# Kernel tuning notes

Hardware: AMD Instinct MI355X
Metric: run time of the kernel (lower is better)

## Reference

```python
import jax, jax.numpy as jnp
import numpy as np

B, N, D, S = 64, 1024, 8, 16
SPARSE_PROB = 0.1


def setup_inputs() -> dict:
    key = jax.random.key(0)
    k_x, k_m, k_ws, k_bd, k_wd, k_bs = jax.random.split(key, 6)
    x = jax.random.normal(k_x, (B, N, D, S), dtype=jnp.float32)
    # conexao='esparsa': (rand < 0.1).float() buffer, exactly like _criar_matriz_conexao
    matriz_conexao = (jax.random.uniform(k_m, (N, N)) < SPARSE_PROB).astype(jnp.float32)
    # Stacked per-neuron parameters of NeuronioDendritico
    w_syn = jax.random.normal(k_ws, (N, D, S), dtype=jnp.float32) * 0.1   # synapse weights
    b_dend = jax.random.normal(k_bd, (N, D), dtype=jnp.float32) * 0.1     # dendrite bias
    w_dend = jax.random.normal(k_wd, (N, D), dtype=jnp.float32) * 0.1     # dendrite->soma weights
    b_soma = jax.random.normal(k_bs, (N,), dtype=jnp.float32) * 0.1       # soma bias
    return {"x": x, "matriz_conexao": matriz_conexao, "w_syn": w_syn,
            "b_dend": b_dend, "w_dend": w_dend, "b_soma": b_soma}


def reference(x, matriz_conexao, w_syn, b_dend, w_dend, b_soma):
    # Connectivity mixing across neurons (conexao != 'densa'):
    # torch.einsum('bids,oi->bods', x, matriz_conexao)
    xm = jnp.einsum('bids,oi->bods', x, matriz_conexao)  # [B, N, D, S]
    # Fused batched version of the Python loop over n_neurons:
    # each dendrite: tanh(sum_s w*x + b)
    dend = jnp.tanh(jnp.einsum('bnds,nds->bnd', xm, w_syn) + b_dend[None])  # [B, N, D]
    # soma: weighted sum of dendritic outputs + bias -> sigmoid spike
    soma = jnp.einsum('bnd,nd->bn', dend, w_dend) + b_soma[None]            # [B, N]
    spikes = jax.nn.sigmoid(soma)
    return spikes
```

## Files before the change

### kernel.cpp

```cpp
#include <hip/hip_runtime.h>
#include <hip/hip_bf16.h>

#define BB 64
#define NN 1024
#define DD 8
#define SS 16
#define DS 128

typedef __attribute__((ext_vector_type(8))) short short8;
typedef __attribute__((ext_vector_type(4))) float floatx4;

typedef __attribute__((address_space(1))) const unsigned int glds_src;
typedef __attribute__((address_space(3))) unsigned int glds_dst;

static __device__ __forceinline__ unsigned short f2bf(float f) {
    unsigned int u = __float_as_uint(f);
    unsigned int r = (u + 0x7FFFu + ((u >> 16) & 1u)) >> 16;
    return (unsigned short)r;
}

__global__ void prepass(const float* __restrict__ x, unsigned short* __restrict__ xT,
                        const float* __restrict__ M, unsigned short* __restrict__ Mb) {
    __shared__ float tile[64 * 68];
    const int t = threadIdx.x;

    if (blockIdx.x < 1024) {
        int i = (blockIdx.x * 256 + t) * 4;
        float4 v = *(const float4*)(M + i);
        unsigned int p0 = (unsigned int)f2bf(v.x) | ((unsigned int)f2bf(v.y) << 16);
        unsigned int p1 = (unsigned int)f2bf(v.z) | ((unsigned int)f2bf(v.w) << 16);
        *(uint2*)(Mb + i) = make_uint2(p0, p1);
        return;
    }

    const int bid = blockIdx.x - 1024;
    const int i0 = (bid & 15) * 64;
    const int c0 = ((bid >> 4) & 1) * 64;
    const int b  = bid >> 5;
    const float* xb = x + (size_t)b * (NN * DS);

#pragma unroll
    for (int jj = 0; jj < 4; ++jj) {
        int il = (t >> 4) + jj * 16;
        int cl = (t & 15) * 4;
        float4 v = *(const float4*)(xb + (size_t)(i0 + il) * DS + c0 + cl);
        *(float4*)(tile + il * 68 + cl) = v;
    }
    __syncthreads();
    int cr  = t >> 2;
    int iq  = (t & 3) * 16;
    int rot = (t & 3) * 2;
    unsigned int p[8];
#pragma unroll
    for (int j = 0; j < 8; ++j) {
        int jp = (j + rot) & 7;
        unsigned short lo = f2bf(tile[(iq + 2 * jp + 0) * 68 + cr]);
        unsigned short hi = f2bf(tile[(iq + 2 * jp + 1) * 68 + cr]);
        p[jp] = (unsigned int)lo | ((unsigned int)hi << 16);
    }
    unsigned short* dst = xT + (size_t)b * (NN * DS) + (size_t)(c0 + cr) * NN + i0 + iq;
    *(uint4*)(dst + 0) = make_uint4(p[0], p[1], p[2], p[3]);
    *(uint4*)(dst + 8) = make_uint4(p[4], p[5], p[6], p[7]);
}

__global__ __launch_bounds__(256, 2) void gemm_fused(
    const unsigned short* __restrict__ Mb,
    const unsigned short* __restrict__ xT,
    const float* __restrict__ w_syn,
    const float* __restrict__ b_dend,
    const float* __restrict__ w_dend,
    const float* __restrict__ b_soma,
    float* __restrict__ out)
{
    __shared__ __align__(16) unsigned short As[128 * 128];
    __shared__ __align__(16) unsigned short Bs[128 * 128];
    __shared__ float ex[128 * 2];

    const int t      = threadIdx.x;
    const int b      = blockIdx.x;
    const int o_base = blockIdx.y * 128;

    const char* AgB = (const char*)(Mb + (size_t)o_base * NN);
    const char* BgB = (const char*)(xT + (size_t)b * (NN * DS));

    const int lane = t & 63;
    const int w    = t >> 6;
    const int wr   = (w >> 1) * 64;
    const int wc   = (w & 1) * 64;
    const int lm   = lane & 15;
    const int kq   = lane >> 4;

    int off[8], ldsb[8];
#pragma unroll
    for (int j = 0; j < 8; ++j) {
        const int row = (w * 8 + j) * 4 + (lane >> 4);
        const int sg  = (lane & 15) ^ (row & 15);
        off[j]  = row * (NN * 2) + sg * 16;
        ldsb[j] = (w * 8 + j) * 1024;
    }

    floatx4 acc[4][4] = {};

    for (int kt = 0; kt < 8; ++kt) {
        const int kb = kt * 256;
        __syncthreads();
#pragma unroll
        for (int j = 0; j < 8; ++j) {
            __builtin_amdgcn_global_load_lds((glds_src*)(AgB + off[j] + kb),
                                             (glds_dst*)((char*)As + ldsb[j]), 16, 0, 0);
            __builtin_amdgcn_global_load_lds((glds_src*)(BgB + off[j] + kb),
                                             (glds_dst*)((char*)Bs + ldsb[j]), 16, 0, 0);
        }
        __syncthreads();
#pragma unroll
        for (int ks = 0; ks < 4; ++ks) {
            short8 af[4], bf[4];
            const int g = (((ks * 4 + kq) ^ lm) * 8);
#pragma unroll
            for (int r = 0; r < 4; ++r)
                af[r] = *(const short8*)(As + (wr + r * 16 + lm) * 128 + g);
#pragma unroll
            for (int c = 0; c < 4; ++c)
                bf[c] = *(const short8*)(Bs + (wc + c * 16 + lm) * 128 + g);
#pragma unroll
            for (int r = 0; r < 4; ++r)
#pragma unroll
                for (int c = 0; c < 4; ++c)
                    acc[r][c] = __builtin_amdgcn_mfma_f32_16x16x32_bf16(af[r], bf[c], acc[r][c], 0, 0, 0);
        }
    }

    float keep[4];
#pragma unroll
    for (int r = 0; r < 4; ++r) {
#pragma unroll
        for (int rg = 0; rg < 4; ++rg) {
            const int o = o_base + wr + r * 16 + kq * 4 + rg;
#pragma unroll
            for (int c = 0; c < 4; ++c) {
                const int d = (w & 1) * 4 + c;
                float p = acc[r][c][rg] * w_syn[o * DS + d * SS + lm];
                p += __shfl_xor(p, 1);
                p += __shfl_xor(p, 2);
                p += __shfl_xor(p, 4);
                p += __shfl_xor(p, 8);
                if (lm == r * 4 + rg) keep[c] = p;
            }
        }
    }
    {
        const int o_loc = wr + (lm >> 2) * 16 + kq * 4 + (lm & 3);
        const int o     = o_base + o_loc;
        float part = 0.f;
#pragma unroll
        for (int c = 0; c < 4; ++c) {
            const int d = (w & 1) * 4 + c;
            float pre = keep[c] + b_dend[o * DD + d];
            part += tanhf(pre) * w_dend[o * DD + d];
        }
        ex[o_loc * 2 + (w & 1)] = part;
    }
    __syncthreads();
    if (t < 128) {
        float soma = ex[t * 2] + ex[t * 2 + 1] + b_soma[o_base + t];
        out[(size_t)b * NN + o_base + t] = 1.f / (1.f + __expf(-soma));
    }
}

extern "C" void kernel_launch(void* const* d_in, const int* in_sizes, int n_in,
                              void* d_out, int out_size, void* d_ws, size_t ws_size,
                              hipStream_t stream) {
    const float* x      = (const float*)d_in[0];
    const float* M      = (const float*)d_in[1];
    const float* w_syn  = (const float*)d_in[2];
    const float* b_dend = (const float*)d_in[3];
    const float* w_dend = (const float*)d_in[4];
    const float* b_soma = (const float*)d_in[5];
    float* out = (float*)d_out;

    unsigned short* xT = (unsigned short*)d_ws;
    unsigned short* Mb = xT + (size_t)BB * NN * DS;

    prepass   <<<dim3(1024 + 2048), 256, 0, stream>>>(x, xT, M, Mb);
    gemm_fused<<<dim3(BB, NN / 128), 256, 0, stream>>>(Mb, xT, w_syn, b_dend, w_dend, b_soma, out);
}
```

Before: 108.5 us.

## Retile fused GEMM to 256x128 with 8 waves and triple-buffered LDS pipeline

Each block now covers 256 output neurons with 512 threads (8 waves in a 2x4 layout), and the K loop uses 64-wide steps with a three-stage LDS buffer fed by async global_load_lds. Loads for stage kt+2 are split into two halves and issued during the MFMA phases, with explicit vmcnt waits, barriers and setprio around the MFMA blocks. The goal is to overlap global loads with matrix math and to halve the re-reads of the per-batch xT tile. This raises LDS use to about 144KB per block and register pressure, which may cut occupancy, and the handwritten wait counts are fragile.

Result: slower. 111.4 us (+2.6%).

```diff
diff --git a/kernel.cpp b/kernel.cpp
--- a/kernel.cpp
+++ b/kernel.cpp
@@ -63,7 +63,7 @@
     *(uint4*)(dst + 8) = make_uint4(p[4], p[5], p[6], p[7]);
 }
 
-__global__ __launch_bounds__(256, 2) void gemm_fused(
+__global__ __launch_bounds__(512, 2) void gemm_fused(
     const unsigned short* __restrict__ Mb,
     const unsigned short* __restrict__ xT,
     const float* __restrict__ w_syn,
@@ -72,97 +72,144 @@
     const float* __restrict__ b_soma,
     float* __restrict__ out)
 {
-    __shared__ __align__(16) unsigned short As[128 * 128];
-    __shared__ __align__(16) unsigned short Bs[128 * 128];
-    __shared__ float ex[128 * 2];
+    __shared__ __align__(16) unsigned short As[3 * 256 * 64];
+    __shared__ __align__(16) unsigned short Bs[3 * 128 * 64];
+    __shared__ float ex[256 * 4];
 
     const int t      = threadIdx.x;
     const int b      = blockIdx.x;
-    const int o_base = blockIdx.y * 128;
+    const int o_base = blockIdx.y * 256;
+
+    const int lane = t & 63;
+    const int w    = t >> 6;
+    const int wm   = w >> 2;
+    const int wn   = w & 3;
+    const int lm   = lane & 15;
+    const int kq   = lane >> 4;
 
     const char* AgB = (const char*)(Mb + (size_t)o_base * NN);
     const char* BgB = (const char*)(xT + (size_t)b * (NN * DS));
 
-    const int lane = t & 63;
-    const int w    = t >> 6;
-    const int wr   = (w >> 1) * 64;
-    const int wc   = (w & 1) * 64;
-    const int lm   = lane & 15;
-    const int kq   = lane >> 4;
-
-    int off[8], ldsb[8];
-#pragma unroll
-    for (int j = 0; j < 8; ++j) {
-        const int row = (w * 8 + j) * 4 + (lane >> 4);
-        const int sg  = (lane & 15) ^ (row & 15);
-        off[j]  = row * (NN * 2) + sg * 16;
-        ldsb[j] = (w * 8 + j) * 1024;
-    }
-
-    floatx4 acc[4][4] = {};
-
-    for (int kt = 0; kt < 8; ++kt) {
-        const int kb = kt * 256;
-        __syncthreads();
-#pragma unroll
-        for (int j = 0; j < 8; ++j) {
-            __builtin_amdgcn_global_load_lds((glds_src*)(AgB + off[j] + kb),
-                                             (glds_dst*)((char*)As + ldsb[j]), 16, 0, 0);
-            __builtin_amdgcn_global_load_lds((glds_src*)(BgB + off[j] + kb),
-                                             (glds_dst*)((char*)Bs + ldsb[j]), 16, 0, 0);
-        }
-        __syncthreads();
-#pragma unroll
-        for (int ks = 0; ks < 4; ++ks) {
-            short8 af[4], bf[4];
-            const int g = (((ks * 4 + kq) ^ lm) * 8);
-#pragma unroll
-            for (int r = 0; r < 4; ++r)
-                af[r] = *(const short8*)(As + (wr + r * 16 + lm) * 128 + g);
-#pragma unroll
-            for (int c = 0; c < 4; ++c)
-                bf[c] = *(const short8*)(Bs + (wc + c * 16 + lm) * 128 + g);
-#pragma unroll
-            for (int r = 0; r < 4; ++r)
-#pragma unroll
-                for (int c = 0; c < 4; ++c)
-                    acc[r][c] = __builtin_amdgcn_mfma_f32_16x16x32_bf16(af[r], bf[c], acc[r][c], 0, 0, 0);
-        }
-    }
-
-    float keep[4];
-#pragma unroll
-    for (int r = 0; r < 4; ++r) {
+    const int r8 = lane >> 3, l8 = lane & 7;
+    const int sg = (l8 ^ r8) * 16;
+    int offA[4], ldsA[4], offB[2], ldsB[2];
+#pragma unroll
+    for (int j = 0; j < 4; ++j) {
+        offA[j] = (w * 32 + j * 8 + r8) * (NN * 2) + sg;
+        ldsA[j] = (w * 32 + j * 8) * 128;
+    }
+#pragma unroll
+    for (int j = 0; j < 2; ++j) {
+        offB[j] = (w * 16 + j * 8 + r8) * (NN * 2) + sg;
+        ldsB[j] = (w * 16 + j * 8) * 128;
+    }
+
+#define STAGE_H0(TT, BUF) do { const int kb_ = (TT) * 128;                                            \
+    __builtin_amdgcn_global_load_lds((glds_src*)(AgB + offA[0] + kb_),                                \
+        (glds_dst*)((char*)As + (BUF) * 32768 + ldsA[0]), 16, 0, 0);                                  \
+    __builtin_amdgcn_global_load_lds((glds_src*)(AgB + offA[1] + kb_),                                \
+        (glds_dst*)((char*)As + (BUF) * 32768 + ldsA[1]), 16, 0, 0);                                  \
+    __builtin_amdgcn_global_load_lds((glds_src*)(BgB + offB[0] + kb_),                                \
+        (glds_dst*)((char*)Bs + (BUF) * 16384 + ldsB[0]), 16, 0, 0);                                  \
+} while (0)
+
+#define STAGE_H1(TT, BUF) do { const int kb_ = (TT) * 128;                                            \
+    __builtin_amdgcn_global_load_lds((glds_src*)(AgB + offA[2] + kb_),                                \
+        (glds_dst*)((char*)As + (BUF) * 32768 + ldsA[2]), 16, 0, 0);                                  \
+    __builtin_amdgcn_global_load_lds((glds_src*)(AgB + offA[3] + kb_),                                \
+        (glds_dst*)((char*)As + (BUF) * 32768 + ldsA[3]), 16, 0, 0);                                  \
+    __builtin_amdgcn_global_load_lds((glds_src*)(BgB + offB[1] + kb_),                                \
+        (glds_dst*)((char*)Bs + (BUF) * 16384 + ldsB[1]), 16, 0, 0);                                  \
+} while (0)
+
+#define NOSTAGE do {} while (0)
+#define VM6  asm volatile("s_waitcnt vmcnt(6)" ::: "memory")
+#define VM0  asm volatile("s_waitcnt vmcnt(0)" ::: "memory")
+#define NOVM do {} while (0)
+
+#define PHASE(KS, BUFC, STMT_STAGE, STMT_VM) do {                                                     \
+    const unsigned short* Ab_ = As + (BUFC) * 16384;                                                  \
+    const unsigned short* Bb_ = Bs + (BUFC) * 8192;                                                   \
+    short8 af_[8], bf_[2];                                                                            \
+    const int gg_ = (((KS) * 4 + kq) ^ (lm & 7)) * 8;                                                 \
+    _Pragma("unroll")                                                                                 \
+    for (int m_ = 0; m_ < 8; ++m_)                                                                    \
+        af_[m_] = *(const short8*)(Ab_ + (wm * 128 + m_ * 16 + lm) * 64 + gg_);                       \
+    _Pragma("unroll")                                                                                 \
+    for (int n_ = 0; n_ < 2; ++n_)                                                                    \
+        bf_[n_] = *(const short8*)(Bb_ + (wn * 32 + n_ * 16 + lm) * 64 + gg_);                        \
+    STMT_STAGE;                                                                                       \
+    STMT_VM;                                                                                          \
+    __builtin_amdgcn_s_barrier();                                                                     \
+    asm volatile("s_waitcnt lgkmcnt(0)" ::: "memory");                                                \
+    __builtin_amdgcn_sched_barrier(0);                                                                \
+    __builtin_amdgcn_s_setprio(1);                                                                    \
+    _Pragma("unroll")                                                                                 \
+    for (int m_ = 0; m_ < 8; ++m_)                                                                    \
+        _Pragma("unroll")                                                                             \
+        for (int n_ = 0; n_ < 2; ++n_)                                                                \
+            acc[m_][n_] = __builtin_amdgcn_mfma_f32_16x16x32_bf16(af_[m_], bf_[n_], acc[m_][n_], 0, 0, 0); \
+    __builtin_amdgcn_s_setprio(0);                                                                    \
+    __builtin_amdgcn_s_barrier();                                                                     \
+} while (0)
+
+    floatx4 acc[8][2] = {};
+
+    STAGE_H0(0, 0); STAGE_H1(0, 0);
+    STAGE_H0(1, 1); STAGE_H1(1, 1);
+    VM6;
+    __builtin_amdgcn_s_barrier();
+
+    for (int kt = 0; kt < 14; ++kt) {
+        const int bufc = kt % 3;
+        const int bufs = (kt + 2) % 3;
+        PHASE(0, bufc, STAGE_H0(kt + 2, bufs), NOVM);
+        PHASE(1, bufc, STAGE_H1(kt + 2, bufs), VM6);
+    }
+    PHASE(0, 2, NOSTAGE, NOVM);
+    PHASE(1, 2, NOSTAGE, VM0);
+    PHASE(0, 0, NOSTAGE, NOVM);
+    PHASE(1, 0, NOSTAGE, NOVM);
+
+#undef PHASE
+#undef STAGE_H0
+#undef STAGE_H1
+
+    float keep[2][2];
+#pragma unroll
+    for (int m = 0; m < 8; ++m) {
 #pragma unroll
         for (int rg = 0; rg < 4; ++rg) {
-            const int o = o_base + wr + r * 16 + kq * 4 + rg;
-#pragma unroll
-            for (int c = 0; c < 4; ++c) {
-                const int d = (w & 1) * 4 + c;
-                float p = acc[r][c][rg] * w_syn[o * DS + d * SS + lm];
+            const int o = o_base + wm * 128 + m * 16 + kq * 4 + rg;
+#pragma unroll
+            for (int n = 0; n < 2; ++n) {
+                const int d = wn * 2 + n;
+                float p = acc[m][n][rg] * w_syn[o * DS + d * SS + lm];
                 p += __shfl_xor(p, 1);
                 p += __shfl_xor(p, 2);
                 p += __shfl_xor(p, 4);
                 p += __shfl_xor(p, 8);
-                if (lm == r * 4 + rg) keep[c] = p;
+                if (lm == (m & 3) * 4 + rg) keep[m >> 2][n] = p;
             }
         }
     }
-    {
-        const int o_loc = wr + (lm >> 2) * 16 + kq * 4 + (lm & 3);
+#pragma unroll
+    for (int mh = 0; mh < 2; ++mh) {
+        const int o_loc = wm * 128 + mh * 64 + (lm >> 2) * 16 + kq * 4 + (lm & 3);
         const int o     = o_base + o_loc;
         float part = 0.f;
 #pragma unroll
-        for (int c = 0; c < 4; ++c) {
-            const int d = (w & 1) * 4 + c;
-            float pre = keep[c] + b_dend[o * DD + d];
+        for (int n = 0; n < 2; ++n) {
+            const int d = wn * 2 + n;
+            float pre = keep[mh][n] + b_dend[o * DD + d];
             part += tanhf(pre) * w_dend[o * DD + d];
         }
-        ex[o_loc * 2 + (w & 1)] = part;
+        ex[o_loc * 4 + wn] = part;
     }
     __syncthreads();
-    if (t < 128) {
-        float soma = ex[t * 2] + ex[t * 2 + 1] + b_soma[o_base + t];
+    if (t < 256) {
+        float soma = ex[t * 4] + ex[t * 4 + 1] + ex[t * 4 + 2] + ex[t * 4 + 3]
+                   + b_soma[o_base + t];
         out[(size_t)b * NN + o_base + t] = 1.f / (1.f + __expf(-soma));
     }
 }
@@ -182,5 +229,5 @@
     unsigned short* Mb = xT + (size_t)BB * NN * DS;
 
     prepass   <<<dim3(1024 + 2048), 256, 0, stream>>>(x, xT, M, Mb);
-    gemm_fused<<<dim3(BB, NN / 128), 256, 0, stream>>>(Mb, xT, w_syn, b_dend, w_dend, b_soma, out);
-}
+    gemm_fused<<<dim3(BB, NN / 256), 512, 0, stream>>>(Mb, xT, w_syn, b_dend, w_dend, b_soma, out);
+}
```

## Load MFMA operands directly from global memory, dropping LDS staging

Applied to the files above, without the earlier changes.

Removes the shared-memory tiles and global_load_lds staging with its per-tile barriers. Each lane now loads its bf16 A and B fragments straight from global memory in a fully unrolled 32-step K loop, and launch bounds are raised to allow three blocks per CU. This removes LDS traffic and synchronization, but it gives up data sharing between waves: each A and B fragment is now fetched by two waves, doubling global/L2 requests. It also adds register pressure from the unrolled loads.

New measurement: 160.7 us. +48.1%, slower.

```diff
diff --git a/kernel.cpp b/kernel.cpp
--- a/kernel.cpp
+++ b/kernel.cpp
@@ -9,9 +9,6 @@
 
 typedef __attribute__((ext_vector_type(8))) short short8;
 typedef __attribute__((ext_vector_type(4))) float floatx4;
-
-typedef __attribute__((address_space(1))) const unsigned int glds_src;
-typedef __attribute__((address_space(3))) unsigned int glds_dst;
 
 static __device__ __forceinline__ unsigned short f2bf(float f) {
     unsigned int u = __float_as_uint(f);
@@ -63,7 +60,7 @@
     *(uint4*)(dst + 8) = make_uint4(p[4], p[5], p[6], p[7]);
 }
 
-__global__ __launch_bounds__(256, 2) void gemm_fused(
+__global__ __launch_bounds__(256, 3) void gemm_fused(
     const unsigned short* __restrict__ Mb,
     const unsigned short* __restrict__ xT,
     const float* __restrict__ w_syn,
@@ -72,16 +69,11 @@
     const float* __restrict__ b_soma,
     float* __restrict__ out)
 {
-    __shared__ __align__(16) unsigned short As[128 * 128];
-    __shared__ __align__(16) unsigned short Bs[128 * 128];
     __shared__ float ex[128 * 2];
 
     const int t      = threadIdx.x;
     const int b      = blockIdx.x;
     const int o_base = blockIdx.y * 128;
-
-    const char* AgB = (const char*)(Mb + (size_t)o_base * NN);
-    const char* BgB = (const char*)(xT + (size_t)b * (NN * DS));
 
     const int lane = t & 63;
     const int w    = t >> 6;
@@ -90,44 +82,32 @@
     const int lm   = lane & 15;
     const int kq   = lane >> 4;
 
-    int off[8], ldsb[8];
+    const char* Ar[4];
+    const char* Bc[4];
 #pragma unroll
-    for (int j = 0; j < 8; ++j) {
-        const int row = (w * 8 + j) * 4 + (lane >> 4);
-        const int sg  = (lane & 15) ^ (row & 15);
-        off[j]  = row * (NN * 2) + sg * 16;
-        ldsb[j] = (w * 8 + j) * 1024;
-    }
+    for (int r = 0; r < 4; ++r)
+        Ar[r] = (const char*)Mb + ((size_t)(o_base + wr + r * 16 + lm) * NN + kq * 8) * 2;
+#pragma unroll
+    for (int c = 0; c < 4; ++c)
+        Bc[c] = (const char*)xT + ((size_t)b * NN * DS + (size_t)(wc + c * 16 + lm) * NN + kq * 8) * 2;
 
     floatx4 acc[4][4] = {};
 
-    for (int kt = 0; kt < 8; ++kt) {
-        const int kb = kt * 256;
-        __syncthreads();
 #pragma unroll
-        for (int j = 0; j < 8; ++j) {
-            __builtin_amdgcn_global_load_lds((glds_src*)(AgB + off[j] + kb),
-                                             (glds_dst*)((char*)As + ldsb[j]), 16, 0, 0);
-            __builtin_amdgcn_global_load_lds((glds_src*)(BgB + off[j] + kb),
-                                             (glds_dst*)((char*)Bs + ldsb[j]), 16, 0, 0);
-        }
-        __syncthreads();
+    for (int k8 = 0; k8 < 32; ++k8) {
+        const int kb = k8 * 64;
+        short8 af[4], bf[4];
 #pragma unroll
-        for (int ks = 0; ks < 4; ++ks) {
-            short8 af[4], bf[4];
-            const int g = (((ks * 4 + kq) ^ lm) * 8);
+        for (int r = 0; r < 4; ++r)
+            af[r] = *(const short8*)(Ar[r] + kb);
 #pragma unroll
-            for (int r = 0; r < 4; ++r)
-                af[r] = *(const short8*)(As + (wr + r * 16 + lm) * 128 + g);
+        for (int c = 0; c < 4; ++c)
+            bf[c] = *(const short8*)(Bc[c] + kb);
+#pragma unroll
+        for (int r = 0; r < 4; ++r)
 #pragma unroll
             for (int c = 0; c < 4; ++c)
-                bf[c] = *(const short8*)(Bs + (wc + c * 16 + lm) * 128 + g);
-#pragma unroll
-            for (int r = 0; r < 4; ++r)
-#pragma unroll
-                for (int c = 0; c < 4; ++c)
-                    acc[r][c] = __builtin_amdgcn_mfma_f32_16x16x32_bf16(af[r], bf[c], acc[r][c], 0, 0, 0);
-        }
+                acc[r][c] = __builtin_amdgcn_mfma_f32_16x16x32_bf16(af[r], bf[c], acc[r][c], 0, 0, 0);
     }
 
     float keep[4];
```
